# Performance work log

Hardware: AMD Instinct MI355X
Metric: run time of the kernel (lower is better)

Reference implementation:

```python
import jax, jax.numpy as jnp
import numpy as np
from functools import partial

GRID = 5  # 224/32 - 2
N_ANCHORS = 3
N_BOX = GRID * GRID * N_ANCHORS  # 75


def _make_anchors():
    # faithful replication of _create_anchors (grid-index cx,cy with pixel-scale w,h)
    scales = [56, 112, 224]
    a = np.zeros((GRID, GRID, N_ANCHORS, 8), np.float32)
    for x in range(GRID):
        for y in range(GRID):
            for k in range(N_ANCHORS):
                w = h = scales[k]
                a[x, y, k] = [x - w // 2, y - h // 2, x + w // 2, y + h // 2, x, y, w, h]
    return jnp.asarray(a)

ANCHORS = _make_anchors()  # [5,5,3,8]: x0,y0,x1,y1,cx,cy,w,h


def conv2d(x, w, b, pad):
    y = jax.lax.conv_general_dilated(x, w, (1, 1), [(pad, pad), (pad, pad)],
                                     dimension_numbers=('NCHW', 'OIHW', 'NCHW'))
    return y + b[None, :, None, None]


def maxpool2(x):
    return jax.lax.reduce_window(x, -jnp.inf, jax.lax.max,
                                 (1, 1, 2, 2), (1, 1, 2, 2), 'VALID')


def deparam_bboxes(rp_reg):
    # rp_reg: [B,5,5,3,4]; anchors broadcast over batch
    aw = ANCHORS[..., 6]; ah = ANCHORS[..., 7]
    ax = ANCHORS[..., 4]; ay = ANCHORS[..., 5]
    cx = rp_reg[..., 0] * aw + ax
    cy = rp_reg[..., 1] * ah + ay
    w = jnp.exp(rp_reg[..., 2]) * aw
    h = jnp.exp(rp_reg[..., 3]) * ah
    return jnp.stack([cx - w / 2, cy - h / 2, cx + w / 2, cy + h / 2], axis=-1)


def _iou_as_written(bi, bj):
    # replicates bb_intersection_over_union EXACTLY, including the missing
    # parentheses bug: inter/areaA + areaB - inter
    xA = jnp.maximum(bi[0], bj[..., 0]); yA = jnp.maximum(bi[1], bj[..., 1])
    xB = jnp.minimum(bi[2], bj[..., 2]); yB = jnp.minimum(bi[3], bj[..., 3])
    inter = jnp.maximum(0.0, xB - xA + 1) * jnp.maximum(0.0, yB - yA + 1)
    areaA = (bi[2] - bi[0] + 1) * (bi[3] - bi[1] + 1)
    areaB = (bj[..., 2] - bj[..., 0] + 1) * (bj[..., 3] - bj[..., 1] + 1)
    return inter / areaA + areaB - inter


def nms_single(boxes, scores, thresh=0.7):
    # boxes [75,4], scores [75]; greedy suppression in score order (vectorized
    # replacement of the O(n^2) Python-loop NMS in _compute_bboxes)
    order = jnp.argsort(-scores)
    b = boxes[order]
    idx = jnp.arange(N_BOX)

    def body(i, keep):
        iou = _iou_as_written(b[i], b)          # [75]
        sup = (idx > i) & (iou > thresh) & keep[i]
        return keep & ~sup

    keep_sorted = jax.lax.fori_loop(0, N_BOX, body, jnp.ones(N_BOX, bool))
    return jnp.zeros(N_BOX, bool).at[order].set(keep_sorted)


def setup_inputs() -> dict:
    key = jax.random.key(0)
    ks = jax.random.split(key, 16)
    B = 32
    inp = {"x": jax.random.normal(ks[0], (B, 3, 224, 224), jnp.float32)}
    chans = [3, 64, 128, 256, 512, 512]
    for i in range(5):
        cin, cout = chans[i], chans[i + 1]
        std = float(np.sqrt(2.0 / (cout * 9)))  # kaiming fan_out, relu
        inp[f"fw{i}"] = jax.random.normal(ks[1 + i], (cout, cin, 3, 3), jnp.float32) * std
        inp[f"fb{i}"] = jnp.zeros((cout,), jnp.float32)
    # RPN heads: normal(0, 0.01), zero bias (per _initialize_rp_weights)
    inp["rpw_w"] = jax.random.normal(ks[6], (512, 512, 3, 3), jnp.float32) * 0.01
    inp["rpw_b"] = jnp.zeros((512,), jnp.float32)
    inp["cls_w"] = jax.random.normal(ks[7], (N_ANCHORS, 512, 1, 1), jnp.float32) * 0.01
    inp["cls_b"] = jnp.zeros((N_ANCHORS,), jnp.float32)
    inp["reg_w"] = jax.random.normal(ks[8], (4 * N_ANCHORS, 512, 1, 1), jnp.float32) * 0.01
    inp["reg_b"] = jnp.zeros((4 * N_ANCHORS,), jnp.float32)
    # classifier2: Linear(512*7*7, 20), normal(0, 0.01)
    inp["fc_w"] = jax.random.normal(ks[9], (20, 512 * 7 * 7), jnp.float32) * 0.01
    inp["fc_b"] = jnp.zeros((20,), jnp.float32)
    return inp


def reference(x, fw0, fb0, fw1, fb1, fw2, fb2, fw3, fb3, fw4, fb4,
              rpw_w, rpw_b, cls_w, cls_b, reg_w, reg_b, fc_w, fc_b):
    B = x.shape[0]
    feat = x
    for w, b in ((fw0, fb0), (fw1, fb1), (fw2, fb2), (fw3, fb3), (fw4, fb4)):
        feat = maxpool2(jax.nn.relu(conv2d(feat, w, b, pad=1)))
    # feat: [B,512,7,7]
    rp512 = jax.nn.relu(conv2d(feat, rpw_w, rpw_b, pad=0))          # [B,512,5,5]
    rp_cls = jax.nn.sigmoid(conv2d(rp512, cls_w, cls_b, pad=0))     # [B,3,5,5]
    rp_reg = conv2d(rp512, reg_w, reg_b, pad=0)                     # [B,12,5,5]
    # faithful to torch .view (row-major reshape, NOT permute)
    rp_cls = rp_cls.reshape(B, GRID, GRID, N_ANCHORS)
    rp_reg = rp_reg.reshape(B, GRID, GRID, N_ANCHORS, 4)
    bboxes = deparam_bboxes(rp_reg)                                 # [B,5,5,3,4]
    keep = jax.vmap(nms_single)(bboxes.reshape(B, N_BOX, 4),
                                rp_cls.reshape(B, N_BOX))           # [B,75] bool
    logits = feat.reshape(B, -1) @ fc_w.T + fc_b                    # [B,20]
    return logits, rp_cls, rp_reg, bboxes, keep
```

## Files before the change

kernel.cpp:

```cpp
#include <hip/hip_runtime.h>
#include <math.h>


#define OFF_LOGITS 0
#define OFF_CLS    640
#define OFF_REG    3040
#define OFF_BOXES  12640
#define OFF_KEEP   22240

constexpr int BATCH = 32;

typedef _Float16 h8 __attribute__((ext_vector_type(8)));
typedef _Float16 h4 __attribute__((ext_vector_type(4)));
typedef float    f4 __attribute__((ext_vector_type(4)));

#define MFMA16(a, b, c) __builtin_amdgcn_mfma_f32_16x16x32_f16(a, b, c, 0, 0, 0)

#if defined(__has_builtin)
#  if __has_builtin(__builtin_amdgcn_global_load_lds)
#    define HAS_GLL 1
#  endif
#endif

__device__ __forceinline__ void stage16(const _Float16* g, _Float16* lbase, int lane) {
#ifdef HAS_GLL
  __builtin_amdgcn_global_load_lds((const __attribute__((address_space(1))) void*)g,
                                   (__attribute__((address_space(3))) void*)lbase,
                                   16, 0, 0);
#else
  *reinterpret_cast<h8*>(lbase + lane * 8) = *reinterpret_cast<const h8*>(g);
#endif
}

constexpr size_t A_OFF = 0;
constexpr size_t B_OFF = 106463232;
constexpr size_t W_OFF = 161579008;
constexpr size_t P_OFF = A_OFF + 8388608;

constexpr int I0_E = 26615808;
constexpr int I1_E = 13778944;
constexpr int I2_E = 7372800;
constexpr int I3_E = 4194304;
constexpr int I4_E = 802816;

__global__ __launch_bounds__(256)
void wcvt(const float* __restrict__ src, _Float16* __restrict__ dHi,
          _Float16* __restrict__ dLo, int COUT, int CIN) {
  const int total = COUT * CIN * 9;
  for (int idx = blockIdx.x * 256 + threadIdx.x; idx < total; idx += gridDim.x * 256) {
    const int co = idx / (CIN * 9);
    const int r = idx % (CIN * 9);
    const int ci = r / 9, tap = r % 9;
    const float v = src[idx];
    const _Float16 h = (_Float16)v;
    const int o = ((tap * (CIN >> 5) + (ci >> 5)) * COUT + co) * 32 + (ci & 31);
    dHi[o] = h;
    dLo[o] = (_Float16)(v - (float)h);
  }
}

__global__ __launch_bounds__(256)
void zero_ring(_Float16* __restrict__ hi, _Float16* __restrict__ lo, int P, int C) {
  const int c8n = C / 8, cells = 4 * P - 4;
  const int tot = 32 * cells * c8n;
  for (int idx = blockIdx.x * 256 + threadIdx.x; idx < tot; idx += gridDim.x * 256) {
    const int c8 = idx % c8n;
    const int cell = (idx / c8n) % cells;
    const int n = idx / (c8n * cells);
    int y, xx;
    if (cell < 2 * P) { y = (cell < P) ? 0 : (P - 1); xx = cell % P; }
    else { const int q = cell - 2 * P; y = 1 + (q >> 1); xx = (q & 1) ? (P - 1) : 0; }
    const long o = ((long)(n * P + y) * P + xx) * C + c8 * 8;
    h8 z = {};
    *reinterpret_cast<h8*>(hi + o) = z;
    *reinterpret_cast<h8*>(lo + o) = z;
  }
}

constexpr int L0_SW   = 0;
constexpr int L0_SB   = 6912;
constexpr int L0_SIN  = 7168;
constexpr int L0_HI   = 7168;
constexpr int L0_LO   = 7168 + 36864;
constexpr int L0_LDS  = 7168 + 73728;

__global__ __launch_bounds__(256)
void conv_l0(const float* __restrict__ x, const float* __restrict__ w0,
             const float* __restrict__ b0, _Float16* __restrict__ outHi,
             _Float16* __restrict__ outLo) {
  const int bid = blockIdx.x;
  const int tx0 = (bid % 7) * 16, ty0 = ((bid / 7) % 7) * 16, n = bid / 49;
  __align__(16) __shared__ char lds[L0_LDS];
  float* sW = (float*)(lds + L0_SW);
  float* sB = (float*)(lds + L0_SB);
  float* sIn = (float*)(lds + L0_SIN);
  const int tid = threadIdx.x;
  for (int idx = tid; idx < 3 * 34 * 34; idx += 256) {
    const int ci = idx / 1156, rem = idx % 1156, r = rem / 34, cc = rem % 34;
    const int y = 2 * ty0 - 1 + r, xx = 2 * tx0 - 1 + cc;
    float v = 0.f;
    if ((unsigned)y < 224u && (unsigned)xx < 224u)
      v = x[((n * 3 + ci) * 224 + y) * 224 + xx];
    sIn[idx] = v;
  }
  for (int idx = tid; idx < 1728; idx += 256) sW[idx] = w0[idx];
  if (tid < 64) sB[tid] = b0[tid];
  __syncthreads();

  const int tpy = tid / 16, tpx = tid % 16;
  float win[3][4][4];
  #pragma unroll
  for (int ci = 0; ci < 3; ++ci)
    #pragma unroll
    for (int dr = 0; dr < 4; ++dr)
      #pragma unroll
      for (int dc = 0; dc < 4; ++dc)
        win[ci][dr][dc] = sIn[ci * 1156 + (2 * tpy + dr) * 34 + (2 * tpx + dc)];
  __syncthreads();

  for (int co4 = 0; co4 < 16; ++co4) {
    h4 hh, ll;
    #pragma unroll
    for (int j = 0; j < 4; ++j) {
      const int co = co4 * 4 + j;
      float a00 = 0.f, a01 = 0.f, a10 = 0.f, a11 = 0.f;
      #pragma unroll
      for (int ci = 0; ci < 3; ++ci)
        #pragma unroll
        for (int ky = 0; ky < 3; ++ky)
          #pragma unroll
          for (int kx = 0; kx < 3; ++kx) {
            const float wv = sW[co * 27 + ci * 9 + ky * 3 + kx];
            a00 = fmaf(win[ci][ky][kx], wv, a00);
            a01 = fmaf(win[ci][ky][kx + 1], wv, a01);
            a10 = fmaf(win[ci][ky + 1][kx], wv, a10);
            a11 = fmaf(win[ci][ky + 1][kx + 1], wv, a11);
          }
      const float p = fmaxf(fmaxf(fmaxf(a00, a01), fmaxf(a10, a11)) + sB[co], 0.f);
      const _Float16 h = (_Float16)p;
      hh[j] = h;
      ll[j] = (_Float16)(p - (float)h);
    }
    *reinterpret_cast<h4*>(lds + L0_HI + tid * 144 + co4 * 8) = hh;
    *reinterpret_cast<h4*>(lds + L0_LO + tid * 144 + co4 * 8) = ll;
  }
  __syncthreads();

  const int tr_half = tid >> 7;
  const int pixrow = (tid & 127) >> 3;
  const int ch8 = (tid & 7) * 8;
  #pragma unroll
  for (int i = 0; i < 8; ++i) {
    const int tr = 2 * i + tr_half;
    const int pix = tr * 16 + pixrow;
    const long ga = ((long)(n * 114 + ty0 + tr + 1) * 114 + tx0 + pixrow + 1) * 64 + ch8;
    *reinterpret_cast<h8*>(outHi + ga) =
        *reinterpret_cast<const h8*>(lds + L0_HI + pix * 144 + ch8 * 2);
    *reinterpret_cast<h8*>(outLo + ga) =
        *reinterpret_cast<const h8*>(lds + L0_LO + pix * 144 + ch8 * 2);
  }
}

template<int CIN, int COUT, int H>
__global__ __launch_bounds__(256, 2)
void convrow2(const _Float16* __restrict__ inHi, const _Float16* __restrict__ inLo,
              const _Float16* __restrict__ wHi, const _Float16* __restrict__ wLo,
              const float* __restrict__ bias, _Float16* __restrict__ outHi,
              _Float16* __restrict__ outLo) {
  constexpr int W = H, Hp = H / 2, Wp = W / 2, PW = W + 2, POW = Wp + 2;
  constexpr int KCH = CIN / 32;
  constexpr int NPH = 3 * KCH;
  constexpr int STG = 136;
  constexpr int XH = (W + 63) / 64;
  __align__(16) __shared__ _Float16 sB[2][2][STG * 32];

  const int tid = threadIdx.x;
  const int lane = tid & 63, wv = tid >> 6;
  const int c = lane & 15, kq = lane >> 4;
  const int cow = (wv & 1) * 64;
  const int spl = (wv >> 1) * 64;
  const int xh = blockIdx.x % XH;
  const int pyn = blockIdx.x / XH;
  const int py = pyn % Hp, n = pyn / Hp;
  const int x0 = xh * 64;

  int gstage[3];
  #pragma unroll
  for (int i = 0; i < 3; ++i) {
    const int sl = i * 64 + tid / 4;
    const int ry = sl & 1;
    int xx = x0 + (sl >> 1);
    if (xx > PW - 1) xx = PW - 1;
    gstage[i] = ((n * (H + 2) + 2 * py + ry) * PW + xx) * CIN +
                (((tid & 3) ^ ((sl >> 1) & 3)) * 8);
  }
  int dsoff[3][4];
  #pragma unroll
  for (int kx = 0; kx < 3; ++kx)
    #pragma unroll
    for (int nt = 0; nt < 4; ++nt) {
      const int r = spl + nt * 16 + c + 2 * kx;
      dsoff[kx][nt] = r * 32 + ((kq ^ ((r >> 1) & 3)) * 8);
    }

  #pragma unroll
  for (int i = 0; i < 2; ++i) {
    stage16(inHi + gstage[i], &sB[0][0][i * 2048 + wv * 512], lane);
    stage16(inLo + gstage[i], &sB[0][1][i * 2048 + wv * 512], lane);
  }
  if (tid < 16) {
    stage16(inHi + gstage[2], &sB[0][0][4096], lane);
    stage16(inLo + gstage[2], &sB[0][1][4096], lane);
  }
  __syncthreads();

  f4 acc[4][4] = {};
  int cur = 0;
  for (int ph = 0; ph < NPH; ++ph) {
    const int ky = ph / KCH, kc = ph % KCH;
    if (ph + 1 < NPH) {
      const int tb2 = ((ph + 1) / KCH) * PW * CIN + ((ph + 1) % KCH) * 32;
      #pragma unroll
      for (int i = 0; i < 2; ++i) {
        stage16(inHi + gstage[i] + tb2, &sB[cur ^ 1][0][i * 2048 + wv * 512], lane);
        stage16(inLo + gstage[i] + tb2, &sB[cur ^ 1][1][i * 2048 + wv * 512], lane);
      }
      if (tid < 16) {
        stage16(inHi + gstage[2] + tb2, &sB[cur ^ 1][0][4096], lane);
        stage16(inLo + gstage[2] + tb2, &sB[cur ^ 1][1][4096], lane);
      }
    }
    #pragma unroll
    for (int kx = 0; kx < 3; ++kx) {
      h8 aH[4], aL[4];
      const long abase = ((long)((ky * 3 + kx) * KCH + kc) * COUT + cow) * 32;
      #pragma unroll
      for (int mt = 0; mt < 4; ++mt) {
        const long ao = abase + (mt * 16 + c) * 32 + kq * 8;
        aH[mt] = *reinterpret_cast<const h8*>(wHi + ao);
        aL[mt] = *reinterpret_cast<const h8*>(wLo + ao);
      }
      h8 bH[4], bL[4];
      #pragma unroll
      for (int nt = 0; nt < 4; ++nt) {
        bH[nt] = *reinterpret_cast<const h8*>(&sB[cur][0][dsoff[kx][nt]]);
        bL[nt] = *reinterpret_cast<const h8*>(&sB[cur][1][dsoff[kx][nt]]);
      }
      __builtin_amdgcn_s_setprio(1);
      #pragma unroll
      for (int mt = 0; mt < 4; ++mt)
        #pragma unroll
        for (int nt = 0; nt < 4; ++nt)
          acc[mt][nt] = MFMA16(aH[mt], bH[nt], acc[mt][nt]);
      #pragma unroll
      for (int mt = 0; mt < 4; ++mt)
        #pragma unroll
        for (int nt = 0; nt < 4; ++nt)
          acc[mt][nt] = MFMA16(aH[mt], bL[nt], acc[mt][nt]);
      #pragma unroll
      for (int mt = 0; mt < 4; ++mt)
        #pragma unroll
        for (int nt = 0; nt < 4; ++nt)
          acc[mt][nt] = MFMA16(aL[mt], bH[nt], acc[mt][nt]);
      __builtin_amdgcn_s_setprio(0);
    }
    __syncthreads();
    cur ^= 1;
  }

  const int r4 = lane >> 4;
  #pragma unroll
  for (int mt = 0; mt < 4; ++mt) {
    const int co0 = cow + mt * 16 + r4 * 4;
    const f4 bi = *reinterpret_cast<const f4*>(bias + co0);
    #pragma unroll
    for (int nt = 0; nt < 4; ++nt) {
      f4 v = acc[mt][nt];
      #pragma unroll
      for (int r = 0; r < 4; ++r) {
        const float m1 = fmaxf(v[r], __shfl_xor(v[r], 1, 64));
        v[r] = fmaxf(m1, __shfl_xor(m1, 2, 64));
      }
      if ((lane & 3) == 0) {
        const int rr = spl + nt * 16 + c;
        const int pxg = xh * 32 + (rr >> 2);
        if (pxg < Wp) {
          h4 hh, ll;
          #pragma unroll
          for (int r = 0; r < 4; ++r) {
            const float p = fmaxf(v[r] + bi[r], 0.f);
            const _Float16 h = (_Float16)p;
            hh[r] = h;
            ll[r] = (_Float16)(p - (float)h);
          }
          const long oa = ((long)((n * (Hp + 2) + py + 1) * POW + pxg + 1)) * COUT + co0;
          *reinterpret_cast<h4*>(outHi + oa) = hh;
          *reinterpret_cast<h4*>(outLo + oa) = ll;
        }
      }
    }
  }
}

template<int CIN, int COUT, int H, int BCO, int BSP, int TG, int KPH, int MODE>
__global__ __launch_bounds__(256, 2)
void convpool(const _Float16* __restrict__ inHi, const _Float16* __restrict__ inLo,
              const _Float16* __restrict__ wHi, const _Float16* __restrict__ wLo,
              const float* __restrict__ bias, _Float16* __restrict__ outHi,
              _Float16* __restrict__ outLo, float* __restrict__ outF) {
  constexpr int W = H, Hp = H / 2, Wp = W / 2, PW = W + 2, POW = Wp + 2;
  constexpr int NCOW = BCO / 64, NSPW = BSP / 64;
  static_assert(NCOW * NSPW == 4, "4 waves");
  constexpr int KCH = CIN / 32;
  constexpr int NCH = TG * KCH;
  constexpr int NPH = NCH / KPH;
  static_assert(NCH % KPH == 0, "even phases");
  static_assert(KPH * 2 * (BSP / 64) == 4, "prologue vmcnt literal = 4");
  constexpr int NISS = BSP / 64;
  constexpr int SPTOT = 32 * H * W;
  constexpr int TSZ = BSP * 32;
  __align__(16) __shared__ _Float16 sB[3 * 2 * KPH * TSZ];
  #define TIDX(buf, hl, j) ((((buf) * 2 + (hl)) * KPH + (j)) * TSZ)

  const int tid = threadIdx.x;
  const int lane = tid & 63, wv = tid >> 6;
  const int c = lane & 15, kq = lane >> 4;
  const int cow = blockIdx.y * BCO + (wv % NCOW) * 64;
  const int spl = (wv / NCOW) * 64;
  const int sblk = blockIdx.x * BSP;
  const int tap0 = (TG == 9) ? 0 : blockIdx.z * TG;

  int gstage[NISS];
  #pragma unroll
  for (int i = 0; i < NISS; ++i) {
    const int sl = i * 64 + tid / 4;
    const int sg = sblk + sl;
    const int ry = sg & 1, tt = sg >> 1;
    const int x = tt % W, u = tt / W;
    const int py = u % Hp, n = u / Hp;
    gstage[i] = ((n * (H + 2) + 2 * py + ry) * PW + x) * CIN +
                (((tid & 3) ^ ((sl >> 1) & 3)) * 8);
  }
  int dsoff[4];
  #pragma unroll
  for (int nt = 0; nt < 4; ++nt) {
    const int row = spl + nt * 16 + c;
    dsoff[nt] = row * 32 + ((kq ^ ((row >> 1) & 3)) * 8);
  }

  #pragma unroll
  for (int pp = 0; pp < 2; ++pp) {
    #pragma unroll
    for (int j = 0; j < KPH; ++j) {
      const int ch = pp * KPH + j;
      const int tap = tap0 + ch / KCH, kc = ch % KCH;
      const int tb = ((tap / 3) * PW + (tap % 3)) * CIN + kc * 32;
      #pragma unroll
      for (int i = 0; i < NISS; ++i) {
        stage16(inHi + gstage[i] + tb, &sB[TIDX(pp, 0, j) + i * 2048 + wv * 512], lane);
        stage16(inLo + gstage[i] + tb, &sB[TIDX(pp, 1, j) + i * 2048 + wv * 512], lane);
      }
    }
  }
  __builtin_amdgcn_sched_barrier(0);
  asm volatile("s_waitcnt vmcnt(4)" ::: "memory");
  __builtin_amdgcn_sched_barrier(0);
  __builtin_amdgcn_s_barrier();
  __builtin_amdgcn_sched_barrier(0);

  f4 acc[4][4] = {};
  for (int ph = 0; ph < NPH; ++ph) {
    const int bp = ph % 3;
    h8 aH[KPH][4], aL[KPH][4];
    #pragma unroll
    for (int j = 0; j < KPH; ++j) {
      const int ch = ph * KPH + j;
      const int tap = tap0 + ch / KCH;
      const int kc = ch % KCH;
      const long abase = ((long)(tap * KCH + kc) * COUT + cow) * 32;
      #pragma unroll
      for (int mt = 0; mt < 4; ++mt) {
        const long ao = abase + (mt * 16 + c) * 32 + kq * 8;
        aH[j][mt] = *reinterpret_cast<const h8*>(wHi + ao);
        aL[j][mt] = *reinterpret_cast<const h8*>(wLo + ao);
      }
    }
    __builtin_amdgcn_sched_barrier(0);
    if (ph + 2 < NPH) {
      const int bs = (ph + 2) % 3;
      #pragma unroll
      for (int j2 = 0; j2 < KPH; ++j2) {
        const int ch2 = (ph + 2) * KPH + j2;
        const int tap2 = tap0 + ch2 / KCH;
        const int tb2 = ((tap2 / 3) * PW + (tap2 % 3)) * CIN + (ch2 % KCH) * 32;
        #pragma unroll
        for (int i = 0; i < NISS; ++i) {
          stage16(inHi + gstage[i] + tb2,
                  &sB[TIDX(bs, 0, j2) + i * 2048 + wv * 512], lane);
          stage16(inLo + gstage[i] + tb2,
                  &sB[TIDX(bs, 1, j2) + i * 2048 + wv * 512], lane);
        }
      }
    }
    __builtin_amdgcn_sched_barrier(0);
    #pragma unroll
    for (int j = 0; j < KPH; ++j) {
      h8 bH[4], bL[4];
      #pragma unroll
      for (int nt = 0; nt < 4; ++nt) {
        bH[nt] = *reinterpret_cast<const h8*>(&sB[TIDX(bp, 0, j) + dsoff[nt]]);
        bL[nt] = *reinterpret_cast<const h8*>(&sB[TIDX(bp, 1, j) + dsoff[nt]]);
      }
      __builtin_amdgcn_s_setprio(1);
      #pragma unroll
      for (int mt = 0; mt < 4; ++mt)
        #pragma unroll
        for (int nt = 0; nt < 4; ++nt)
          acc[mt][nt] = MFMA16(aH[j][mt], bH[nt], acc[mt][nt]);
      #pragma unroll
      for (int mt = 0; mt < 4; ++mt)
        #pragma unroll
        for (int nt = 0; nt < 4; ++nt)
          acc[mt][nt] = MFMA16(aH[j][mt], bL[nt], acc[mt][nt]);
      #pragma unroll
      for (int mt = 0; mt < 4; ++mt)
        #pragma unroll
        for (int nt = 0; nt < 4; ++nt)
          acc[mt][nt] = MFMA16(aL[j][mt], bH[nt], acc[mt][nt]);
      __builtin_amdgcn_s_setprio(0);
    }
    __builtin_amdgcn_sched_barrier(0);
    __builtin_amdgcn_s_barrier();
    __builtin_amdgcn_sched_barrier(0);
  }
  #undef TIDX

  const int r4 = lane >> 4;
  if (MODE == 1) {
    #pragma unroll
    for (int mt = 0; mt < 4; ++mt) {
      const int co0 = cow + mt * 16 + r4 * 4;
      #pragma unroll
      for (int nt = 0; nt < 4; ++nt) {
        const int s = sblk + spl + nt * 16 + c;
        *reinterpret_cast<f4*>(outF + ((long)blockIdx.z * SPTOT + s) * COUT + co0) =
            acc[mt][nt];
      }
    }
  } else {
    #pragma unroll
    for (int mt = 0; mt < 4; ++mt) {
      const int co0 = cow + mt * 16 + r4 * 4;
      const f4 bi = *reinterpret_cast<const f4*>(bias + co0);
      #pragma unroll
      for (int nt = 0; nt < 4; ++nt) {
        f4 v = acc[mt][nt];
        #pragma unroll
        for (int r = 0; r < 4; ++r) {
          const float m1 = fmaxf(v[r], __shfl_xor(v[r], 1, 64));
          v[r] = fmaxf(m1, __shfl_xor(m1, 2, 64));
        }
        if ((lane & 3) == 0) {
          const int s = sblk + spl + nt * 16 + c;
          const int ps = s >> 2;
          const int n = ps / (Hp * Wp), rem = ps % (Hp * Wp);
          const int py = rem / Wp, px = rem % Wp;
          h4 hh, ll;
          #pragma unroll
          for (int r = 0; r < 4; ++r) {
            const float p = fmaxf(v[r] + bi[r], 0.f);
            const _Float16 h = (_Float16)p;
            hh[r] = h;
            ll[r] = (_Float16)(p - (float)h);
          }
          const long oa = ((long)((n * (Hp + 2) + py + 1) * POW + px + 1)) * COUT + co0;
          *reinterpret_cast<h4*>(outHi + oa) = hh;
          *reinterpret_cast<h4*>(outLo + oa) = ll;
        }
      }
    }
  }
}

__global__ __launch_bounds__(256)
void l4_finish(const float* __restrict__ part, const float* __restrict__ bias,
               _Float16* __restrict__ I4h, _Float16* __restrict__ I4l,
               float* __restrict__ feat) {
  const int t = blockIdx.x * 256 + threadIdx.x;
  if (t >= 1568 * 128) return;
  const int co0 = (t % 128) * 4, p = t / 128;
  f4 m;
  #pragma unroll
  for (int q = 0; q < 4; ++q) {
    const long s = 4L * p + q;
    f4 v = *reinterpret_cast<const f4*>(part + s * 512 + co0);
    v += *reinterpret_cast<const f4*>(part + (6272 + s) * 512 + co0);
    v += *reinterpret_cast<const f4*>(part + (12544 + s) * 512 + co0);
    if (q == 0) m = v;
    else {
      #pragma unroll
      for (int r = 0; r < 4; ++r) m[r] = fmaxf(m[r], v[r]);
    }
  }
  const f4 bi = *reinterpret_cast<const f4*>(bias + co0);
  h4 hh, ll;
  const int n = p / 49, pix = p % 49;
  #pragma unroll
  for (int r = 0; r < 4; ++r) {
    const float pv = fmaxf(m[r] + bi[r], 0.f);
    const _Float16 h = (_Float16)pv;
    hh[r] = h;
    ll[r] = (_Float16)(pv - (float)h);
    feat[((long)(n * 512 + co0 + r)) * 49 + pix] = pv;
  }
  *reinterpret_cast<h4*>(I4h + (long)p * 512 + co0) = hh;
  *reinterpret_cast<h4*>(I4l + (long)p * 512 + co0) = ll;
}

__global__ __launch_bounds__(256)
void rpn_partial(const _Float16* __restrict__ inHi, const _Float16* __restrict__ inLo,
                 const _Float16* __restrict__ wHi, const _Float16* __restrict__ wLo,
                 float* __restrict__ part) {
  const int lane = threadIdx.x & 63, wv = threadIdx.x >> 6;
  const int cow = blockIdx.y * 128 + wv * 32;
  const int sblk = blockIdx.x * 64;
  const int tap = blockIdx.z, ky = tap / 3, kx = tap % 3;
  const int c = lane & 15, kq = lane >> 4;

  int baseB[4];
  #pragma unroll
  for (int nt = 0; nt < 4; ++nt) {
    int s = sblk + nt * 16 + c;
    if (s > 799) s = 799;
    const int n = s / 25, pix = s % 25, py = pix / 5, px = pix % 5;
    baseB[nt] = ((n * 7 + py + ky) * 7 + px + kx) * 512;
  }

  f4 acc[2][4] = {};
  for (int kch = 0; kch < 16; ++kch) {
    h8 aH[2], aL[2], bH[4], bL[4];
    const long abase = ((long)(tap * 16 + kch) * 512 + cow) * 32;
    #pragma unroll
    for (int mt = 0; mt < 2; ++mt) {
      const long ao = abase + (mt * 16 + c) * 32 + kq * 8;
      aH[mt] = *reinterpret_cast<const h8*>(wHi + ao);
      aL[mt] = *reinterpret_cast<const h8*>(wLo + ao);
    }
    #pragma unroll
    for (int nt = 0; nt < 4; ++nt) {
      const int bo = baseB[nt] + kch * 32 + kq * 8;
      bH[nt] = *reinterpret_cast<const h8*>(inHi + bo);
      bL[nt] = *reinterpret_cast<const h8*>(inLo + bo);
    }
    #pragma unroll
    for (int mt = 0; mt < 2; ++mt)
      #pragma unroll
      for (int nt = 0; nt < 4; ++nt)
        acc[mt][nt] = MFMA16(aH[mt], bH[nt], acc[mt][nt]);
    #pragma unroll
    for (int mt = 0; mt < 2; ++mt)
      #pragma unroll
      for (int nt = 0; nt < 4; ++nt)
        acc[mt][nt] = MFMA16(aH[mt], bL[nt], acc[mt][nt]);
    #pragma unroll
    for (int mt = 0; mt < 2; ++mt)
      #pragma unroll
      for (int nt = 0; nt < 4; ++nt)
        acc[mt][nt] = MFMA16(aL[mt], bH[nt], acc[mt][nt]);
  }

  const int r4 = lane >> 4;
  #pragma unroll
  for (int mt = 0; mt < 2; ++mt) {
    const int co0 = cow + mt * 16 + r4 * 4;
    #pragma unroll
    for (int nt = 0; nt < 4; ++nt) {
      const int s = sblk + nt * 16 + c;
      if (s < 800)
        *reinterpret_cast<f4*>(part + ((long)tap * 800 + s) * 512 + co0) = acc[mt][nt];
    }
  }
}

__global__ __launch_bounds__(256)
void rpn_finish(const float* __restrict__ part, const float* __restrict__ bias,
                float* __restrict__ rp512) {
  const int t = blockIdx.x * 256 + threadIdx.x;
  if (t >= 800 * 128) return;
  const int co0 = (t % 128) * 4, s = t / 128;
  f4 acc = *reinterpret_cast<const f4*>(bias + co0);
  #pragma unroll
  for (int g = 0; g < 9; ++g)
    acc += *reinterpret_cast<const f4*>(part + ((long)g * 800 + s) * 512 + co0);
  f4 o;
  #pragma unroll
  for (int r = 0; r < 4; ++r) o[r] = fmaxf(acc[r], 0.f);
  *reinterpret_cast<f4*>(rp512 + (long)s * 512 + co0) = o;
}

__global__ __launch_bounds__(256)
void heads_kernel(const float* __restrict__ rp512,
                  const float* __restrict__ cls_w, const float* __restrict__ cls_b,
                  const float* __restrict__ reg_w, const float* __restrict__ reg_b,
                  float* __restrict__ out) {
  const int idx = blockIdx.x * 256 + threadIdx.x;
  if (idx >= 32 * 25 * 15) return;
  const int o = idx % 15, pix = (idx / 15) % 25, n = idx / 375;
  const float* __restrict__ ip = rp512 + ((long)(n * 25 + pix)) * 512;
  const float* __restrict__ wvp = (o < 3) ? (cls_w + o * 512) : (reg_w + (o - 3) * 512);
  float acc = 0.f;
  for (int k = 0; k < 512; k += 4) {
    const f4 a = *reinterpret_cast<const f4*>(ip + k);
    const f4 b = *reinterpret_cast<const f4*>(wvp + k);
    acc = fmaf(a[0], b[0], acc); acc = fmaf(a[1], b[1], acc);
    acc = fmaf(a[2], b[2], acc); acc = fmaf(a[3], b[3], acc);
  }
  if (o < 3) {
    acc += cls_b[o];
    out[OFF_CLS + n * 75 + o * 25 + pix] = 1.f / (1.f + expf(-acc));
  } else {
    acc += reg_b[o - 3];
    out[OFF_REG + n * 300 + (o - 3) * 25 + pix] = acc;
  }
}

__global__ __launch_bounds__(256)
void fc_kernel(const float* __restrict__ feat, const float* __restrict__ fw,
               const float* __restrict__ fb, float* __restrict__ out) {
  const int n = blockIdx.x, j = blockIdx.y;
  const float* __restrict__ ip = feat + (long)n * 25088;
  const float* __restrict__ wj = fw + (long)j * 25088;
  float acc = 0.f;
  for (int k = threadIdx.x * 4; k < 25088; k += 1024) {
    const f4 a = *reinterpret_cast<const f4*>(ip + k);
    const f4 b = *reinterpret_cast<const f4*>(wj + k);
    acc = fmaf(a[0], b[0], acc); acc = fmaf(a[1], b[1], acc);
    acc = fmaf(a[2], b[2], acc); acc = fmaf(a[3], b[3], acc);
  }
  #pragma unroll
  for (int m = 32; m >= 1; m >>= 1) acc += __shfl_xor(acc, m, 64);
  __shared__ float red[4];
  const int wv = threadIdx.x >> 6;
  if ((threadIdx.x & 63) == 0) red[wv] = acc;
  __syncthreads();
  if (threadIdx.x == 0)
    out[OFF_LOGITS + n * 20 + j] = red[0] + red[1] + red[2] + red[3] + fb[j];
}

__global__ __launch_bounds__(128)
void bbox_nms_kernel(float* __restrict__ out) {
  const int n = blockIdx.x;
  const int t = threadIdx.x;
  __shared__ float bx0[75], by0[75], bx1[75], by1[75], area[75], sc[75];
  __shared__ int rank_s[75], order_s[75], keep_s[75];

  if (t < 75) {
    const int g1 = t / 15, g2 = (t / 3) % 5, a = t % 3;
    const float aw = (a == 0) ? 56.f : (a == 1 ? 112.f : 224.f);
    const float r0 = out[OFF_REG + n * 300 + 4 * t + 0];
    const float r1 = out[OFF_REG + n * 300 + 4 * t + 1];
    const float r2 = out[OFF_REG + n * 300 + 4 * t + 2];
    const float r3 = out[OFF_REG + n * 300 + 4 * t + 3];
    const float cx = r0 * aw + (float)g1;
    const float cy = r1 * aw + (float)g2;
    const float w_ = expf(r2) * aw;
    const float h_ = expf(r3) * aw;
    const float x0 = cx - 0.5f * w_, y0 = cy - 0.5f * h_;
    const float x1 = cx + 0.5f * w_, y1 = cy + 0.5f * h_;
    bx0[t] = x0; by0[t] = y0; bx1[t] = x1; by1[t] = y1;
    area[t] = (x1 - x0 + 1.f) * (y1 - y0 + 1.f);
    out[OFF_BOXES + n * 300 + 4 * t + 0] = x0;
    out[OFF_BOXES + n * 300 + 4 * t + 1] = y0;
    out[OFF_BOXES + n * 300 + 4 * t + 2] = x1;
    out[OFF_BOXES + n * 300 + 4 * t + 3] = y1;
    sc[t] = out[OFF_CLS + n * 75 + t];
    keep_s[t] = 1;
  }
  __syncthreads();
  if (t < 75) {
    const float si = sc[t];
    int rk = 0;
    for (int j = 0; j < 75; ++j) {
      const float sj = sc[j];
      rk += (sj > si) || (sj == si && j < t);
    }
    rank_s[t] = rk;
    order_s[rk] = t;
  }
  __syncthreads();
  for (int i = 0; i < 74; ++i) {
    if (keep_s[i]) {
      const int bi = order_s[i];
      if (t > i && t < 75) {
        const int bj = order_s[t];
        const float xA = fmaxf(bx0[bi], bx0[bj]);
        const float yA = fmaxf(by0[bi], by0[bj]);
        const float xB = fminf(bx1[bi], bx1[bj]);
        const float yB = fminf(by1[bi], by1[bj]);
        const float inter = fmaxf(0.f, xB - xA + 1.f) * fmaxf(0.f, yB - yA + 1.f);
        const float iou = inter / area[bi] + area[bj] - inter;
        if (iou > 0.7f) keep_s[t] = 0;
      }
    }
    __syncthreads();
  }
  if (t < 75) out[OFF_KEEP + n * 75 + t] = keep_s[rank_s[t]] ? 1.f : 0.f;
}

extern "C" void kernel_launch(void* const* d_in, const int* in_sizes, int n_in,
                              void* d_out, int out_size, void* d_ws, size_t ws_size,
                              hipStream_t stream) {
  (void)in_sizes; (void)n_in; (void)out_size; (void)ws_size;
  const float* x     = (const float*)d_in[0];
  const float* fw0   = (const float*)d_in[1];
  const float* fb0   = (const float*)d_in[2];
  const float* fw1   = (const float*)d_in[3];
  const float* fb1   = (const float*)d_in[4];
  const float* fw2   = (const float*)d_in[5];
  const float* fb2   = (const float*)d_in[6];
  const float* fw3   = (const float*)d_in[7];
  const float* fb3   = (const float*)d_in[8];
  const float* fw4   = (const float*)d_in[9];
  const float* fb4   = (const float*)d_in[10];
  const float* rpw_w = (const float*)d_in[11];
  const float* rpw_b = (const float*)d_in[12];
  const float* cls_w = (const float*)d_in[13];
  const float* cls_b = (const float*)d_in[14];
  const float* reg_w = (const float*)d_in[15];
  const float* reg_b = (const float*)d_in[16];
  const float* fc_w  = (const float*)d_in[17];
  const float* fc_b  = (const float*)d_in[18];
  float* out = (float*)d_out;
  char* ws = (char*)d_ws;

  _Float16* I0h = (_Float16*)(ws + A_OFF);
  _Float16* I0l = I0h + I0_E;
  _Float16* I1h = (_Float16*)(ws + B_OFF);
  _Float16* I1l = I1h + I1_E;
  _Float16* I2h = (_Float16*)(ws + A_OFF);
  _Float16* I2l = I2h + I2_E;
  _Float16* I3h = (_Float16*)(ws + B_OFF);
  _Float16* I3l = I3h + I3_E;
  _Float16* I4h = (_Float16*)(ws + A_OFF);
  _Float16* I4l = I4h + I4_E;
  float* feat  = (float*)(ws + A_OFF + (size_t)I4_E * 4);
  float* rp512 = (float*)(ws + A_OFF + (size_t)I4_E * 4 + 3211264);
  float* part  = (float*)(ws + P_OFF);

  _Float16* w1h = (_Float16*)(ws + W_OFF);                _Float16* w1l = w1h + 73728;
  _Float16* w2h = (_Float16*)(ws + W_OFF + 294912);       _Float16* w2l = w2h + 294912;
  _Float16* w3h = (_Float16*)(ws + W_OFF + 1474560);      _Float16* w3l = w3h + 1179648;
  _Float16* w4h = (_Float16*)(ws + W_OFF + 6193152);      _Float16* w4l = w4h + 2359296;
  _Float16* wrh = (_Float16*)(ws + W_OFF + 15630336);     _Float16* wrl = wrh + 2359296;

  wcvt<<<(73728 + 255) / 256, 256, 0, stream>>>(fw1, w1h, w1l, 128, 64);
  wcvt<<<(294912 + 255) / 256, 256, 0, stream>>>(fw2, w2h, w2l, 256, 128);
  wcvt<<<(1179648 + 255) / 256, 256, 0, stream>>>(fw3, w3h, w3l, 512, 256);
  wcvt<<<(2359296 + 255) / 256, 256, 0, stream>>>(fw4, w4h, w4l, 512, 512);
  wcvt<<<(2359296 + 255) / 256, 256, 0, stream>>>(rpw_w, wrh, wrl, 512, 512);

  zero_ring<<<512, 256, 0, stream>>>(I0h, I0l, 114, 64);
  zero_ring<<<512, 256, 0, stream>>>(I1h, I1l, 58, 128);

  conv_l0<<<32 * 49, 256, 0, stream>>>(x, fw0, fb0, I0h, I0l);

  convrow2<64, 128, 112><<<dim3(32 * 56 * 2, 1, 1), 256, 0, stream>>>(
      I0h, I0l, w1h, w1l, fb1, I1h, I1l);
  zero_ring<<<512, 256, 0, stream>>>(I2h, I2l, 30, 256);
  convpool<128, 256, 56, 256, 64, 9, 2, 0><<<dim3(1568, 1, 1), 256, 0, stream>>>(
      I1h, I1l, w2h, w2l, fb2, I2h, I2l, nullptr);
  zero_ring<<<512, 256, 0, stream>>>(I3h, I3l, 16, 512);
  convpool<256, 512, 28, 256, 64, 9, 2, 0><<<dim3(392, 2, 1), 256, 0, stream>>>(
      I2h, I2l, w3h, w3l, fb3, I3h, I3l, nullptr);
  convpool<512, 512, 14, 256, 64, 3, 2, 1><<<dim3(98, 2, 3), 256, 0, stream>>>(
      I3h, I3l, w4h, w4l, nullptr, nullptr, nullptr, part);
  l4_finish<<<(1568 * 128 + 255) / 256, 256, 0, stream>>>(part, fb4, I4h, I4l, feat);

  rpn_partial<<<dim3(13, 4, 9), 256, 0, stream>>>(I4h, I4l, wrh, wrl, part);
  rpn_finish<<<(800 * 128 + 255) / 256, 256, 0, stream>>>(part, rpw_b, rp512);

  heads_kernel<<<(12000 + 255) / 256, 256, 0, stream>>>(rp512, cls_w, cls_b, reg_w, reg_b, out);
  fc_kernel<<<dim3(32, 20), 256, 0, stream>>>(feat, fc_w, fc_b, out);
  bbox_nms_kernel<<<BATCH, 128, 0, stream>>>(out);
}
```

Baseline: 884.2 us.

## Generalize row-pair conv kernel and use it for layers two and three

The row-based conv+pool kernel is templated on x-halves, output-channel groups per block, and staging size. Layers 2 and 3 now use it instead of the generic convpool kernel, with blockIdx.y splitting output channels. For layer 3 the four waves all cover different output channels over one 64-pixel span. The aim is better operand reuse and fewer wasted staged rows for the smaller spatial sizes. The trade-off is different occupancy and padding waste, for example 56- or 28-wide rows staged inside 64-pixel tiles.

```diff
diff --git a/kernel.cpp b/kernel.cpp
--- a/kernel.cpp
+++ b/kernel.cpp
@@ -161,32 +161,34 @@
   }
 }
 
-template<int CIN, int COUT, int H>
+template<int CIN, int COUT, int H, int XH, int NCOW, int STG, int SARR>
 __global__ __launch_bounds__(256, 2)
-void convrow2(const _Float16* __restrict__ inHi, const _Float16* __restrict__ inLo,
-              const _Float16* __restrict__ wHi, const _Float16* __restrict__ wLo,
-              const float* __restrict__ bias, _Float16* __restrict__ outHi,
-              _Float16* __restrict__ outLo) {
+void convrow(const _Float16* __restrict__ inHi, const _Float16* __restrict__ inLo,
+             const _Float16* __restrict__ wHi, const _Float16* __restrict__ wLo,
+             const float* __restrict__ bias, _Float16* __restrict__ outHi,
+             _Float16* __restrict__ outLo) {
   constexpr int W = H, Hp = H / 2, Wp = W / 2, PW = W + 2, POW = Wp + 2;
   constexpr int KCH = CIN / 32;
   constexpr int NPH = 3 * KCH;
-  constexpr int STG = 136;
-  constexpr int XH = (W + 63) / 64;
-  __align__(16) __shared__ _Float16 sB[2][2][STG * 32];
+  constexpr int NSPW = 4 / NCOW;
+  constexpr int NFULL = STG / 64;
+  constexpr int TAIL = STG % 64;
+  static_assert(NSPW * 64 + 3 < STG + 1, "staged rows cover shifted reads");
+  __align__(16) __shared__ _Float16 sB[2][2][SARR * 32];
 
   const int tid = threadIdx.x;
   const int lane = tid & 63, wv = tid >> 6;
   const int c = lane & 15, kq = lane >> 4;
-  const int cow = (wv & 1) * 64;
-  const int spl = (wv >> 1) * 64;
+  const int cow = blockIdx.y * (NCOW * 64) + (wv % NCOW) * 64;
+  const int spl = (wv / NCOW) * 64;
   const int xh = blockIdx.x % XH;
   const int pyn = blockIdx.x / XH;
   const int py = pyn % Hp, n = pyn / Hp;
   const int x0 = xh * 64;
 
-  int gstage[3];
-  #pragma unroll
-  for (int i = 0; i < 3; ++i) {
+  int gstage[NFULL + 1];
+  #pragma unroll
+  for (int i = 0; i < NFULL + 1; ++i) {
     const int sl = i * 64 + tid / 4;
     const int ry = sl & 1;
     int xx = x0 + (sl >> 1);
@@ -204,13 +206,13 @@
     }
 
   #pragma unroll
-  for (int i = 0; i < 2; ++i) {
+  for (int i = 0; i < NFULL; ++i) {
     stage16(inHi + gstage[i], &sB[0][0][i * 2048 + wv * 512], lane);
     stage16(inLo + gstage[i], &sB[0][1][i * 2048 + wv * 512], lane);
   }
-  if (tid < 16) {
-    stage16(inHi + gstage[2], &sB[0][0][4096], lane);
-    stage16(inLo + gstage[2], &sB[0][1][4096], lane);
+  if (TAIL && tid < TAIL * 4) {
+    stage16(inHi + gstage[NFULL], &sB[0][0][NFULL * 2048], lane);
+    stage16(inLo + gstage[NFULL], &sB[0][1][NFULL * 2048], lane);
   }
   __syncthreads();
 
@@ -221,13 +223,13 @@
     if (ph + 1 < NPH) {
       const int tb2 = ((ph + 1) / KCH) * PW * CIN + ((ph + 1) % KCH) * 32;
       #pragma unroll
-      for (int i = 0; i < 2; ++i) {
+      for (int i = 0; i < NFULL; ++i) {
         stage16(inHi + gstage[i] + tb2, &sB[cur ^ 1][0][i * 2048 + wv * 512], lane);
         stage16(inLo + gstage[i] + tb2, &sB[cur ^ 1][1][i * 2048 + wv * 512], lane);
       }
-      if (tid < 16) {
-        stage16(inHi + gstage[2] + tb2, &sB[cur ^ 1][0][4096], lane);
-        stage16(inLo + gstage[2] + tb2, &sB[cur ^ 1][1][4096], lane);
+      if (TAIL && tid < TAIL * 4) {
+        stage16(inHi + gstage[NFULL] + tb2, &sB[cur ^ 1][0][NFULL * 2048], lane);
+        stage16(inLo + gstage[NFULL] + tb2, &sB[cur ^ 1][1][NFULL * 2048], lane);
       }
     }
     #pragma unroll
@@ -764,14 +766,14 @@
 
   conv_l0<<<32 * 49, 256, 0, stream>>>(x, fw0, fb0, I0h, I0l);
 
-  convrow2<64, 128, 112><<<dim3(32 * 56 * 2, 1, 1), 256, 0, stream>>>(
+  convrow<64, 128, 112, 2, 2, 132, 136><<<dim3(32 * 56 * 2, 1), 256, 0, stream>>>(
       I0h, I0l, w1h, w1l, fb1, I1h, I1l);
   zero_ring<<<512, 256, 0, stream>>>(I2h, I2l, 30, 256);
-  convpool<128, 256, 56, 256, 64, 9, 2, 0><<<dim3(1568, 1, 1), 256, 0, stream>>>(
-      I1h, I1l, w2h, w2l, fb2, I2h, I2l, nullptr);
+  convrow<128, 256, 56, 1, 2, 132, 136><<<dim3(32 * 28, 2), 256, 0, stream>>>(
+      I1h, I1l, w2h, w2l, fb2, I2h, I2l);
   zero_ring<<<512, 256, 0, stream>>>(I3h, I3l, 16, 512);
-  convpool<256, 512, 28, 256, 64, 9, 2, 0><<<dim3(392, 2, 1), 256, 0, stream>>>(
-      I2h, I2l, w3h, w3l, fb3, I3h, I3l, nullptr);
+  convrow<256, 512, 28, 1, 4, 68, 72><<<dim3(32 * 14, 2), 256, 0, stream>>>(
+      I2h, I2l, w3h, w3l, fb3, I3h, I3l);
   convpool<512, 512, 14, 256, 64, 3, 2, 1><<<dim3(98, 2, 3), 256, 0, stream>>>(
       I3h, I3l, w4h, w4l, nullptr, nullptr, nullptr, part);
   l4_finish<<<(1568 * 128 + 255) / 256, 256, 0, stream>>>(part, fb4, I4h, I4l, feat);
```

New measurement: 865.9 us. 1.02x faster.
